# Performance work log

Measured on AMD Instinct MI355X. Metric: run time of the kernel, lower is better.

## Reference

```python
import jax, jax.numpy as jnp
import numpy as np

N_NODES = 50000
N_EDGES = 800000
IN_C = 32
HID = 64
N_LAYERS = 3
EDGE_HID = 128
OUT_C = 1
N_GRAPHS = 8


def setup_inputs() -> dict:
    key = jax.random.key(0)
    ks = jax.random.split(key, 32)
    x = jax.random.normal(ks[0], (N_NODES, IN_C), dtype=jnp.float32)
    # edges with src != dst so that PyG's remove_self_loops is a no-op
    src = jax.random.randint(ks[1], (N_EDGES,), 0, N_NODES)
    off = jax.random.randint(ks[2], (N_EDGES,), 1, N_NODES)
    dst = (src + off) % N_NODES
    edge_index = jnp.stack([src, dst]).astype(jnp.int32)
    batch = jnp.sort(jax.random.randint(ks[3], (N_NODES,), 0, N_GRAPHS)).astype(jnp.int32)
    inp = {"x": x, "edge_index": edge_index, "batch": batch}
    i = 4
    for l in range(N_LAYERS):
        din = IN_C if l == 0 else HID
        s = 1.0 / float(np.sqrt(din))
        inp[f"Wl{l}"] = jax.random.normal(ks[i], (din, HID), dtype=jnp.float32) * s; i += 1
        inp[f"bl{l}"] = jnp.zeros((HID,), jnp.float32)
        inp[f"Wr{l}"] = jax.random.normal(ks[i], (din, HID), dtype=jnp.float32) * s; i += 1
        inp[f"br{l}"] = jnp.zeros((HID,), jnp.float32)
        inp[f"att{l}"] = jax.random.normal(ks[i], (HID,), dtype=jnp.float32) * (1.0 / float(np.sqrt(HID))); i += 1
        inp[f"res{l}"] = jax.random.normal(ks[i], (din, HID), dtype=jnp.float32) * s; i += 1
        inp[f"bias{l}"] = jnp.zeros((HID,), jnp.float32)
        inp[f"lng{l}"] = jnp.ones((HID,), jnp.float32)
        inp[f"lnb{l}"] = jnp.zeros((HID,), jnp.float32)
    efd = 3 * HID
    inp["W1"] = jax.random.normal(ks[i], (efd, EDGE_HID), dtype=jnp.float32) * (1.0 / float(np.sqrt(efd))); i += 1
    inp["b1"] = jnp.zeros((EDGE_HID,), jnp.float32)
    inp["W2"] = jax.random.normal(ks[i], (EDGE_HID, OUT_C), dtype=jnp.float32) * (1.0 / float(np.sqrt(EDGE_HID))); i += 1
    inp["b2"] = jnp.zeros((OUT_C,), jnp.float32)
    return inp


def _gatv2_layer(x, src, dst, Wl, bl, Wr, br, att, resW, bias):
    # GATv2Conv (heads=1, share_weights=False, residual=True, add_self_loops handled by caller)
    n = x.shape[0]
    xl = x @ Wl + bl  # source transform  [N, C]
    xr = x @ Wr + br  # target transform  [N, C]
    e = jax.nn.leaky_relu(xl[src] + xr[dst], 0.2)  # [E, C]
    logits = e @ att                               # [E]
    m = jax.ops.segment_max(logits, dst, num_segments=n)
    ex = jnp.exp(logits - m[dst])
    denom = jax.ops.segment_sum(ex, dst, num_segments=n)
    alpha = ex / denom[dst]                        # edge softmax over incoming edges
    out = jax.ops.segment_sum(alpha[:, None] * xl[src], dst, num_segments=n)
    return out + x @ resW + bias


def _layernorm(h, g, b):
    mu = h.mean(-1, keepdims=True)
    var = h.var(-1, keepdims=True)
    return (h - mu) * jax.lax.rsqrt(var + 1e-5) * g + b


def reference(x, edge_index, batch,
              Wl0, bl0, Wr0, br0, att0, res0, bias0, lng0, lnb0,
              Wl1, bl1, Wr1, br1, att1, res1, bias1, lng1, lnb1,
              Wl2, bl2, Wr2, br2, att2, res2, bias2, lng2, lnb2,
              W1, b1, W2, b2):
    n = x.shape[0]
    loop = jnp.arange(n, dtype=edge_index.dtype)
    src = jnp.concatenate([edge_index[0], loop])  # add self loops
    dst = jnp.concatenate([edge_index[1], loop])
    layers = [(Wl0, bl0, Wr0, br0, att0, res0, bias0, lng0, lnb0),
              (Wl1, bl1, Wr1, br1, att1, res1, bias1, lng1, lnb1),
              (Wl2, bl2, Wr2, br2, att2, res2, bias2, lng2, lnb2)]
    h = x
    for (Wl, bl, Wr, br, att, resW, bias, g, b) in layers:
        h = _gatv2_layer(h, src, dst, Wl, bl, Wr, br, att, resW, bias)
        h = jax.nn.relu(_layernorm(h, g, b))
    node_repr = h
    gc = jax.ops.segment_sum(node_repr, batch, num_segments=N_GRAPHS)  # global_add_pool
    s, d = edge_index[0], edge_index[1]
    edge_feat = jnp.concatenate([node_repr[s], node_repr[d], gc[batch[s]]], axis=-1)  # [E, 3*HID]
    return jax.nn.relu(edge_feat @ W1 + b1) @ W2 + b2
```

## Files before the change

kernel.cpp:

```cpp
#include <hip/hip_runtime.h>
#include <math.h>

typedef float floatx2 __attribute__((ext_vector_type(2)));
typedef float floatx4 __attribute__((ext_vector_type(4)));
typedef short bf16x8 __attribute__((ext_vector_type(8)));
typedef _Float16 halfx2 __attribute__((ext_vector_type(2)));

#define NODE_MASK 0x07FFFFFF
#define LOG2E 1.4426950408889634f

__device__ __forceinline__ float wave_sum(float v){
#pragma unroll
  for (int m = 1; m < 64; m <<= 1) v += __shfl_xor(v, m, 64);
  return v;
}

__device__ __forceinline__ unsigned short bf16_of(float a){
  unsigned ua = __float_as_uint(a);
  ua = (ua + 0x7FFFu + ((ua >> 16) & 1u)) >> 16;
  return (unsigned short)ua;
}
__device__ __forceinline__ unsigned pack_bf16(float a, float b){
  unsigned ua = __float_as_uint(a), ub = __float_as_uint(b);
  ua = (ua + 0x7FFFu + ((ua >> 16) & 1u)) >> 16;
  ub = (ub + 0x7FFFu + ((ub >> 16) & 1u)) >> 16;
  return ua | (ub << 16);
}
__device__ __forceinline__ float2 unpack_bf16(unsigned p){
  float2 r;
  r.x = __uint_as_float(p << 16);
  r.y = __uint_as_float(p & 0xFFFF0000u);
  return r;
}
__device__ __forceinline__ bf16x8 to_bf16x8(float4 a, float4 b){
  bf16x8 r;
  r[0]=(short)bf16_of(a.x); r[1]=(short)bf16_of(a.y);
  r[2]=(short)bf16_of(a.z); r[3]=(short)bf16_of(a.w);
  r[4]=(short)bf16_of(b.x); r[5]=(short)bf16_of(b.y);
  r[6]=(short)bf16_of(b.z); r[7]=(short)bf16_of(b.w);
  return r;
}
__device__ __forceinline__ halfx2 f22h2(float a, float b){
  auto r = __builtin_amdgcn_cvt_pkrtz(a, b);
  return *(halfx2*)&r;
}
__device__ __forceinline__ float fdot2h(halfx2 a, halfx2 b, float c){
  return __builtin_amdgcn_fdot2(a, b, c, false);
}

__global__ void k_deg_rank(const int* __restrict__ dst, int* __restrict__ deg,
                           int* __restrict__ rank, int e){
  int i = (blockIdx.x*blockDim.x + threadIdx.x) * 4;
  if (i + 3 < e){
    int4 d4 = *(const int4*)&dst[i];
    int4 r4;
    r4.x = atomicAdd(&deg[d4.x], 1);
    r4.y = atomicAdd(&deg[d4.y], 1);
    r4.z = atomicAdd(&deg[d4.z], 1);
    r4.w = atomicAdd(&deg[d4.w], 1);
    *(int4*)&rank[i] = r4;
  } else {
    for (int j = i; j < e; ++j) rank[j] = atomicAdd(&deg[dst[j]], 1);
  }
}

__global__ void k_scan_a(const int* __restrict__ deg, int* __restrict__ rowptr,
                         int* __restrict__ bsum, int n){
  __shared__ int sm[256];
  int i = blockIdx.x*256 + threadIdx.x;
  int v = (i < n) ? (deg[i] + 1) : 0;
  sm[threadIdx.x] = v; __syncthreads();
#pragma unroll
  for (int off = 1; off < 256; off <<= 1){
    int t = (threadIdx.x >= off) ? sm[threadIdx.x - off] : 0;
    __syncthreads();
    sm[threadIdx.x] += t;
    __syncthreads();
  }
  if (i < n) rowptr[i] = sm[threadIdx.x] - v;
  if (threadIdx.x == 255) bsum[blockIdx.x] = sm[255];
}

__global__ void k_scan_b(int* __restrict__ bsum, int* __restrict__ rowptr, int nb, int n){
  __shared__ int sm[256];
  int t = threadIdx.x;
  int v = (t < nb) ? bsum[t] : 0;
  sm[t] = v; __syncthreads();
#pragma unroll
  for (int off = 1; off < 256; off <<= 1){
    int x = (t >= off) ? sm[t - off] : 0;
    __syncthreads();
    sm[t] += x;
    __syncthreads();
  }
  if (t < nb) bsum[t] = sm[t] - v;
  if (t == 255) rowptr[n] = sm[255];
}

__global__ void k_scan_c_selfloop(int* __restrict__ rowptr, const int* __restrict__ bsum,
                                  int* __restrict__ csr,
                                  const int* __restrict__ batch,
                                  float* __restrict__ gc, int n){
  int i = blockIdx.x*256 + threadIdx.x;
  if (i < n){
    int r = rowptr[i] + bsum[blockIdx.x];
    rowptr[i] = r;
    csr[r] = i | (batch[i] << 27);
  }
  if (blockIdx.x == 0){
    gc[threadIdx.x] = 0.f;
    gc[threadIdx.x + 256] = 0.f;
  }
}

__global__ void k_scatter(const int* __restrict__ src, const int* __restrict__ dst,
                          const int* __restrict__ batch,
                          const int* __restrict__ rowptr, const int* __restrict__ rank,
                          int* __restrict__ csr, int* __restrict__ eidA, int e){
  int i = (blockIdx.x*blockDim.x + threadIdx.x) * 4;
  if (i + 3 < e){
    int4 s4 = *(const int4*)&src[i];
    int4 d4 = *(const int4*)&dst[i];
    int4 r4 = *(const int4*)&rank[i];
    int p0 = rowptr[d4.x] + 1 + r4.x;
    int p1 = rowptr[d4.y] + 1 + r4.y;
    int p2 = rowptr[d4.z] + 1 + r4.z;
    int p3 = rowptr[d4.w] + 1 + r4.w;
    csr[p0] = s4.x | (batch[s4.x] << 27);
    csr[p1] = s4.y | (batch[s4.y] << 27);
    csr[p2] = s4.z | (batch[s4.z] << 27);
    csr[p3] = s4.w | (batch[s4.w] << 27);
    eidA[p0] = i;
    eidA[p1] = i + 1;
    eidA[p2] = i + 2;
    eidA[p3] = i + 3;
  } else {
    for (int j = i; j < e; ++j){
      int d = dst[j], sv = src[j];
      int pos = rowptr[d] + 1 + rank[j];
      csr[pos] = sv | (batch[sv] << 27);
      eidA[pos] = j;
    }
  }
}

template<int K>
__global__ __launch_bounds__(256)
void k_node_transform(const float* __restrict__ h,
                      const float* __restrict__ Wl, const float* __restrict__ bl,
                      const float* __restrict__ Wr, const float* __restrict__ br,
                      const float* __restrict__ Wres, const float* __restrict__ bias,
                      unsigned short* __restrict__ xl8, float* __restrict__ xr,
                      float* __restrict__ res, int n){
  const int KH = K / 32;
  int lane = threadIdx.x & 63;
  int nt   = threadIdx.x >> 6;
  int nn = lane & 15, q = lane >> 4;
  int m0 = blockIdx.x * 64;
  if (m0 >= n) return;
  bf16x8 Af[4][KH];
#pragma unroll
  for (int t = 0; t < 4; ++t){
#pragma unroll
    for (int kh = 0; kh < KH; ++kh){
      int node = min(m0 + t*16 + nn, n - 1);
      const float* hp = h + (size_t)node*K + kh*32 + q*8;
      Af[t][kh] = to_bf16x8(*(const float4*)hp, *(const float4*)(hp + 4));
    }
  }
  int n0 = nt * 16;
  for (int sel = 0; sel < 3; ++sel){
    const float* Wp = (sel == 0) ? Wl : (sel == 1) ? Wr : Wres;
    const float* bp = (sel == 0) ? bl : (sel == 1) ? br : bias;
    bf16x8 Bf[KH];
#pragma unroll
    for (int kh = 0; kh < KH; ++kh){
#pragma unroll
      for (int j = 0; j < 8; ++j)
        Bf[kh][j] = (short)bf16_of(Wp[(kh*32 + q*8 + j)*64 + n0 + nn]);
    }
    float bv = bp[n0 + nn];
#pragma unroll
    for (int t = 0; t < 4; ++t){
      floatx4 acc = {bv, bv, bv, bv};
#pragma unroll
      for (int kh = 0; kh < KH; ++kh)
        acc = __builtin_amdgcn_mfma_f32_16x16x32_bf16(Af[t][kh], Bf[kh], acc, 0, 0, 0);
      int nodeb = m0 + t*16 + q*4;
      if (sel == 0){
#pragma unroll
        for (int reg = 0; reg < 4; ++reg){
          float v = acc[reg];
          float p = __shfl_xor(v, 1, 64);
          int node = nodeb + reg;
          if (!(nn & 1) && node < n)
            xl8[(size_t)node*32 + ((n0 + nn) >> 1)] =
              (unsigned short)__builtin_amdgcn_cvt_pk_fp8_f32(v, p, 0, false);
        }
      } else {
        float* op = (sel == 1) ? xr : res;
#pragma unroll
        for (int reg = 0; reg < 4; ++reg){
          int node = nodeb + reg;
          if (node < n) op[(size_t)node*64 + n0 + nn] = acc[reg];
        }
      }
    }
  }
}

__global__ void k_gat_edge(const uint2* __restrict__ xl_u2, const float* __restrict__ xr,
                           const float* __restrict__ att,
                           const float* __restrict__ lng, const float* __restrict__ lnb,
                           const int* __restrict__ rowptr, const int* __restrict__ csr,
                           float* __restrict__ hio, int n){
  int node = (blockIdx.x*blockDim.x + threadIdx.x) >> 6;
  int lane = threadIdx.x & 63;
  if (node >= n) return;
  int sub = lane >> 3;
  int l   = lane & 7;
  size_t base = (size_t)node*64 + 8*l;
  float4 xr0 = *(const float4*)&xr[base];
  float4 xr1 = *(const float4*)&xr[base + 4];
  float4 at0f = *(const float4*)&att[8*l];
  float4 at1f = *(const float4*)&att[8*l + 4];
  halfx2 xh0 = f22h2(xr0.x, xr0.y), xh1 = f22h2(xr0.z, xr0.w);
  halfx2 xh2 = f22h2(xr1.x, xr1.y), xh3 = f22h2(xr1.z, xr1.w);
  halfx2 at0 = f22h2(at0f.x*LOG2E, at0f.y*LOG2E);
  halfx2 at1 = f22h2(at0f.z*LOG2E, at0f.w*LOG2E);
  halfx2 at2 = f22h2(at1f.x*LOG2E, at1f.y*LOG2E);
  halfx2 at3 = f22h2(at1f.z*LOG2E, at1f.w*LOG2E);
  halfx2 z2  = {(_Float16)0.f, (_Float16)0.f};
  halfx2 c02 = {(_Float16)0.2f, (_Float16)0.2f};
  int p0 = rowptr[node], p1 = rowptr[node+1];
  int deg = p1 - p0;
  int sreg = csr[p0 + min(lane, deg-1)];
  int rounds = (deg + 7) >> 3;
  float dsum = 0.f;
  float a0=0.f,a1=0.f,a2=0.f,a3=0.f,a4=0.f,a5=0.f,a6=0.f,a7=0.f;
  int e0 = sub;
  bool v0 = e0 < deg;
  int s0 = __shfl(sreg, v0 ? e0 : 0, 64) & NODE_MASK;
  uint2 x0 = xl_u2[(size_t)s0*8 + l];
  int e1 = 8 + sub;
  bool v1 = e1 < deg;
  uint2 x1 = x0;
  if (rounds > 1){
    int s1 = __shfl(sreg, v1 ? e1 : 0, 64) & NODE_MASK;
    x1 = xl_u2[(size_t)s1*8 + l];
  }
  for (int r = 0; r < rounds; ++r){
    int en = 8*(r+2) + sub;
    bool vn = en < deg;
    uint2 xn = x0;
    if (r + 2 < rounds){
      int sn;
      if (en < 64) sn = __shfl(sreg, vn ? en : 0, 64);
      else         sn = csr[p0 + (vn ? en : 0)];
      sn &= NODE_MASK;
      xn = xl_u2[(size_t)sn*8 + l];
    }
    floatx2 p01 = __builtin_amdgcn_cvt_pk_f32_fp8(x0.x, false);
    floatx2 p23 = __builtin_amdgcn_cvt_pk_f32_fp8(x0.x, true);
    floatx2 p45 = __builtin_amdgcn_cvt_pk_f32_fp8(x0.y, false);
    floatx2 p67 = __builtin_amdgcn_cvt_pk_f32_fp8(x0.y, true);
    halfx2 v0h = f22h2(p01.x, p01.y) + xh0;
    halfx2 v1h = f22h2(p23.x, p23.y) + xh1;
    halfx2 v2h = f22h2(p45.x, p45.y) + xh2;
    halfx2 v3h = f22h2(p67.x, p67.y) + xh3;
    halfx2 lr0 = __builtin_elementwise_min(v0h, z2) * c02 + __builtin_elementwise_max(v0h, z2);
    halfx2 lr1 = __builtin_elementwise_min(v1h, z2) * c02 + __builtin_elementwise_max(v1h, z2);
    halfx2 lr2 = __builtin_elementwise_min(v2h, z2) * c02 + __builtin_elementwise_max(v2h, z2);
    halfx2 lr3 = __builtin_elementwise_min(v3h, z2) * c02 + __builtin_elementwise_max(v3h, z2);
    float partial = fdot2h(lr3, at3, fdot2h(lr2, at2, fdot2h(lr1, at1, fdot2h(lr0, at0, 0.f))));
#pragma unroll
    for (int mm = 1; mm < 8; mm <<= 1) partial += __shfl_xor(partial, mm, 64);
    float w = v0 ? exp2f(partial) : 0.f;
    dsum += w;
    a0 = fmaf(w, p01.x, a0);
    a1 = fmaf(w, p01.y, a1);
    a2 = fmaf(w, p23.x, a2);
    a3 = fmaf(w, p23.y, a3);
    a4 = fmaf(w, p45.x, a4);
    a5 = fmaf(w, p45.y, a5);
    a6 = fmaf(w, p67.x, a6);
    a7 = fmaf(w, p67.y, a7);
    x0 = x1; v0 = v1;
    x1 = xn; v1 = vn;
  }
#pragma unroll
  for (int off = 8; off < 64; off <<= 1){
    dsum += __shfl_xor(dsum, off, 64);
    a0 += __shfl_xor(a0, off, 64);
    a1 += __shfl_xor(a1, off, 64);
    a2 += __shfl_xor(a2, off, 64);
    a3 += __shfl_xor(a3, off, 64);
    a4 += __shfl_xor(a4, off, 64);
    a5 += __shfl_xor(a5, off, 64);
    a6 += __shfl_xor(a6, off, 64);
    a7 += __shfl_xor(a7, off, 64);
  }
  float4 r0 = *(const float4*)&hio[base];
  float4 r1 = *(const float4*)&hio[base + 4];
  float inv = __builtin_amdgcn_rcpf(dsum);
  float o0 = fmaf(a0, inv, r0.x);
  float o1 = fmaf(a1, inv, r0.y);
  float o2 = fmaf(a2, inv, r0.z);
  float o3 = fmaf(a3, inv, r0.w);
  float o4 = fmaf(a4, inv, r1.x);
  float o5 = fmaf(a5, inv, r1.y);
  float o6 = fmaf(a6, inv, r1.z);
  float o7 = fmaf(a7, inv, r1.w);
  float mean = wave_sum(o0+o1+o2+o3+o4+o5+o6+o7) * (1.f/512.f);
  float d0 = o0-mean, d1 = o1-mean, d2 = o2-mean, d3 = o3-mean;
  float d4 = o4-mean, d5 = o5-mean, d6 = o6-mean, d7 = o7-mean;
  float var = wave_sum(d0*d0+d1*d1+d2*d2+d3*d3+d4*d4+d5*d5+d6*d6+d7*d7) * (1.f/512.f);
  float rstd = rsqrtf(var + 1e-5f);
  if (sub == 0){
    float4 lg0 = *(const float4*)&lng[8*l];
    float4 lg1 = *(const float4*)&lng[8*l + 4];
    float4 lb0 = *(const float4*)&lnb[8*l];
    float4 lb1 = *(const float4*)&lnb[8*l + 4];
    float4 out0, out1;
    out0.x = fmaxf(fmaf(d0*rstd, lg0.x, lb0.x), 0.f);
    out0.y = fmaxf(fmaf(d1*rstd, lg0.y, lb0.y), 0.f);
    out0.z = fmaxf(fmaf(d2*rstd, lg0.z, lb0.z), 0.f);
    out0.w = fmaxf(fmaf(d3*rstd, lg0.w, lb0.w), 0.f);
    out1.x = fmaxf(fmaf(d4*rstd, lg1.x, lb1.x), 0.f);
    out1.y = fmaxf(fmaf(d5*rstd, lg1.y, lb1.y), 0.f);
    out1.z = fmaxf(fmaf(d6*rstd, lg1.z, lb1.z), 0.f);
    out1.w = fmaxf(fmaf(d7*rstd, lg1.w, lb1.w), 0.f);
    *(float4*)&hio[base] = out0;
    *(float4*)&hio[base + 4] = out1;
  }
}

__global__ void k_pool(const float* __restrict__ h, const int* __restrict__ batch,
                       float* __restrict__ gc, int n){
  int wid  = (blockIdx.x*blockDim.x + threadIdx.x) >> 6;
  int lane = threadIdx.x & 63;
  int n0 = wid*64;
  if (n0 >= n) return;
  int n1 = min(n0+64, n);
  int curg = batch[n0];
  float s = 0.f;
  for (int i = n0; i < n1; ++i){
    int g = batch[i];
    if (g != curg){ atomicAdd(&gc[curg*64+lane], s); s = 0.f; curg = g; }
    s += h[(size_t)i*64 + lane];
  }
  atomicAdd(&gc[curg*64+lane], s);
}

__global__ void k_graph_proj(const float* __restrict__ gc, const float* __restrict__ W1,
                             const float* __restrict__ b1, unsigned* __restrict__ Gh){
  int g = threadIdx.x >> 7;
  int j = threadIdx.x & 127;
  float a = b1[j];
#pragma unroll 8
  for (int k = 0; k < 64; ++k) a = fmaf(gc[g*64+k], W1[(128+k)*128 + j], a);
  float p = __shfl_xor(a, 1, 64);
  if (!(j & 1)){
    halfx2 hv = f22h2(a, p);
    Gh[g*64 + (j >> 1)] = *(unsigned*)&hv;
  }
}

__global__ __launch_bounds__(256)
void k_node_proj(const float* __restrict__ nr, const float* __restrict__ W1,
                 unsigned short* __restrict__ Au16, unsigned* __restrict__ Bu, int n){
  int lane = threadIdx.x & 63;
  int wave = threadIdx.x >> 6;
  int nn = lane & 15, q = lane >> 4;
  int m0 = blockIdx.x * 64;
  if (m0 >= n) return;
  bf16x8 Af[4][2];
#pragma unroll
  for (int t = 0; t < 4; ++t){
#pragma unroll
    for (int kh = 0; kh < 2; ++kh){
      int node = min(m0 + t*16 + nn, n - 1);
      const float* hp = nr + (size_t)node*64 + kh*32 + q*8;
      Af[t][kh] = to_bf16x8(*(const float4*)hp, *(const float4*)(hp + 4));
    }
  }
  for (int half = 0; half < 2; ++half){
#pragma unroll
    for (int ni = 0; ni < 2; ++ni){
      int nt = wave + ni*4;
      int n0 = nt * 16;
      bf16x8 Bf[2];
#pragma unroll
      for (int kh = 0; kh < 2; ++kh){
#pragma unroll
        for (int j = 0; j < 8; ++j)
          Bf[kh][j] = (short)bf16_of(W1[(half*64 + kh*32 + q*8 + j)*128 + n0 + nn]);
      }
#pragma unroll
      for (int t = 0; t < 4; ++t){
        floatx4 acc = {0.f, 0.f, 0.f, 0.f};
#pragma unroll
        for (int kh = 0; kh < 2; ++kh)
          acc = __builtin_amdgcn_mfma_f32_16x16x32_bf16(Af[t][kh], Bf[kh], acc, 0, 0, 0);
        int nodeb = m0 + t*16 + q*4;
#pragma unroll
        for (int reg = 0; reg < 4; ++reg){
          float v = acc[reg];
          float p = __shfl_xor(v, 1, 64);
          int node = nodeb + reg;
          if (!(nn & 1) && node < n){
            int j = (n0 + nn) >> 1;
            if (half == 0)
              Au16[(size_t)node*64 + j] =
                (unsigned short)__builtin_amdgcn_cvt_pk_fp8_f32(v, p, 0, false);
            else
              Bu[(size_t)node*64 + j] = pack_bf16(v, p);
          }
        }
      }
    }
  }
}

__global__ void k_edge_out_csr(const uint4* __restrict__ Au4, const uint4* __restrict__ Bu4,
                               const unsigned* __restrict__ Gh,
                               const int* __restrict__ rowptr, const int* __restrict__ csr,
                               const int* __restrict__ eidA,
                               const float* __restrict__ W2, const float* __restrict__ b2,
                               float* __restrict__ out, int n){
  int node = (blockIdx.x*blockDim.x + threadIdx.x) >> 6;
  int lane = threadIdx.x & 63;
  if (node >= n) return;
  int sub = lane >> 3;
  int l   = lane & 7;
  int p0 = rowptr[node];
  int deg2 = rowptr[node+1] - p0 - 1;
  if (deg2 <= 0) return;
  int idx = p0 + 1 + min(lane, deg2-1);
  int sreg = csr[idx];
  int ereg = eidA[idx];
  uint4 ba = Bu4[(size_t)node*16 + 2*l];
  uint4 bb = Bu4[(size_t)node*16 + 2*l + 1];
  float2 t0 = unpack_bf16(ba.x), t1 = unpack_bf16(ba.y);
  float2 t2 = unpack_bf16(ba.z), t3 = unpack_bf16(ba.w);
  float2 t4 = unpack_bf16(bb.x), t5 = unpack_bf16(bb.y);
  float2 t6 = unpack_bf16(bb.z), t7 = unpack_bf16(bb.w);
  halfx2 bh0 = f22h2(t0.x, t0.y), bh1 = f22h2(t1.x, t1.y);
  halfx2 bh2 = f22h2(t2.x, t2.y), bh3 = f22h2(t3.x, t3.y);
  halfx2 bh4 = f22h2(t4.x, t4.y), bh5 = f22h2(t5.x, t5.y);
  halfx2 bh6 = f22h2(t6.x, t6.y), bh7 = f22h2(t7.x, t7.y);
  float4 w0 = *(const float4*)&W2[16*l];
  float4 w1 = *(const float4*)&W2[16*l + 4];
  float4 w2 = *(const float4*)&W2[16*l + 8];
  float4 w3 = *(const float4*)&W2[16*l + 12];
  halfx2 wh0 = f22h2(w0.x, w0.y), wh1 = f22h2(w0.z, w0.w);
  halfx2 wh2 = f22h2(w1.x, w1.y), wh3 = f22h2(w1.z, w1.w);
  halfx2 wh4 = f22h2(w2.x, w2.y), wh5 = f22h2(w2.z, w2.w);
  halfx2 wh6 = f22h2(w3.x, w3.y), wh7 = f22h2(w3.z, w3.w);
  halfx2 z2 = {(_Float16)0.f, (_Float16)0.f};
  float b2v = b2[0];
  int rounds = (deg2 + 7) >> 3;
  int e0 = sub;
  bool v0 = e0 < deg2;
  int q0 = v0 ? e0 : 0;
  int c0 = __shfl(sreg, q0, 64);
  int id0 = __shfl(ereg, q0, 64);
  uint4 A0 = Au4[(size_t)(c0 & NODE_MASK)*8 + l];
  int e1 = 8 + sub;
  bool v1 = e1 < deg2;
  int c1 = c0, id1 = id0; uint4 A1 = A0;
  if (rounds > 1){
    int q1 = v1 ? e1 : 0;
    c1 = __shfl(sreg, q1, 64);
    id1 = __shfl(ereg, q1, 64);
    A1 = Au4[(size_t)(c1 & NODE_MASK)*8 + l];
  }
  for (int r = 0; r < rounds; ++r){
    int en = 8*(r+2) + sub;
    bool vn = en < deg2;
    int cn = c0, idn = id0; uint4 An = A0;
    if (r + 2 < rounds){
      int qn = vn ? en : 0;
      if (en < 64){ cn = __shfl(sreg, qn, 64); idn = __shfl(ereg, qn, 64); }
      else        { cn = csr[p0 + 1 + qn];     idn = eidA[p0 + 1 + qn]; }
      An = Au4[(size_t)(cn & NODE_MASK)*8 + l];
    }
    int g = ((unsigned)c0) >> 27;
    const uint4* gp = (const uint4*)(Gh + g*64 + 8*l);
    uint4 g0 = gp[0], g1 = gp[1];
    halfx2 gh0 = *(halfx2*)&g0.x, gh1 = *(halfx2*)&g0.y;
    halfx2 gh2 = *(halfx2*)&g0.z, gh3 = *(halfx2*)&g0.w;
    halfx2 gh4 = *(halfx2*)&g1.x, gh5 = *(halfx2*)&g1.y;
    halfx2 gh6 = *(halfx2*)&g1.z, gh7 = *(halfx2*)&g1.w;
    floatx2 a01 = __builtin_amdgcn_cvt_pk_f32_fp8(A0.x, false);
    floatx2 a23 = __builtin_amdgcn_cvt_pk_f32_fp8(A0.x, true);
    floatx2 a45 = __builtin_amdgcn_cvt_pk_f32_fp8(A0.y, false);
    floatx2 a67 = __builtin_amdgcn_cvt_pk_f32_fp8(A0.y, true);
    floatx2 a89 = __builtin_amdgcn_cvt_pk_f32_fp8(A0.z, false);
    floatx2 aab = __builtin_amdgcn_cvt_pk_f32_fp8(A0.z, true);
    floatx2 acd = __builtin_amdgcn_cvt_pk_f32_fp8(A0.w, false);
    floatx2 aef = __builtin_amdgcn_cvt_pk_f32_fp8(A0.w, true);
    halfx2 h0 = __builtin_elementwise_max(f22h2(a01.x, a01.y) + bh0 + gh0, z2);
    halfx2 h1 = __builtin_elementwise_max(f22h2(a23.x, a23.y) + bh1 + gh1, z2);
    halfx2 h2 = __builtin_elementwise_max(f22h2(a45.x, a45.y) + bh2 + gh2, z2);
    halfx2 h3 = __builtin_elementwise_max(f22h2(a67.x, a67.y) + bh3 + gh3, z2);
    halfx2 h4 = __builtin_elementwise_max(f22h2(a89.x, a89.y) + bh4 + gh4, z2);
    halfx2 h5 = __builtin_elementwise_max(f22h2(aab.x, aab.y) + bh5 + gh5, z2);
    halfx2 h6 = __builtin_elementwise_max(f22h2(acd.x, acd.y) + bh6 + gh6, z2);
    halfx2 h7 = __builtin_elementwise_max(f22h2(aef.x, aef.y) + bh7 + gh7, z2);
    float part = fdot2h(h7, wh7, fdot2h(h6, wh6, fdot2h(h5, wh5, fdot2h(h4, wh4,
                 fdot2h(h3, wh3, fdot2h(h2, wh2, fdot2h(h1, wh1, fdot2h(h0, wh0, 0.f))))))));
#pragma unroll
    for (int mm = 1; mm < 8; mm <<= 1) part += __shfl_xor(part, mm, 64);
    if (l == 0 && v0) out[id0] = part + b2v;
    c0 = c1; id0 = id1; A0 = A1; v0 = v1;
    c1 = cn; id1 = idn; A1 = An; v1 = vn;
  }
}

extern "C" void kernel_launch(void* const* d_in, const int* in_sizes, int n_in,
                              void* d_out, int out_size, void* d_ws, size_t ws_size,
                              hipStream_t stream){
  const float* x     = (const float*)d_in[0];
  const int*   ei    = (const int*)d_in[1];
  const int*   batch = (const int*)d_in[2];
  const int N = in_sizes[2];
  const int E = in_sizes[1] / 2;
  const int* src = ei;
  const int* dst = ei + E;

  unsigned* W = (unsigned*)d_ws;
  const size_t N16 = (size_t)N * 16;
  const size_t N32 = (size_t)N * 32;
  const size_t N64 = (size_t)N * 64;
  unsigned short* xl8 = (unsigned short*)W;
  float* xr = (float*)(W + N16);
  float* hE = (float*)(W + N16 + N64);
  float* hD = (float*)(W + N16 + 2*N64);
  unsigned short* Au16 = (unsigned short*)W;
  unsigned* Bu = W + N32;
  int* rowptr = (int*)(W + N16 + 3*N64);
  int* deg    = rowptr + (N + 16);
  int* csr    = deg + N;
  int* rank   = csr + (N + E);
  int* eidA   = rank + E;
  float* gc   = (float*)(eidA + (N + E));
  unsigned* Gh = (unsigned*)(gc + 512);
  int* bsum   = (int*)(Gh + 512);

  const int NB = (N + 255) / 256;
  const int NT64 = (N + 63) / 64;

  (void)hipMemsetAsync(deg, 0, (size_t)N*4, stream);
  k_deg_rank <<<(E/4+255)/256, 256, 0, stream>>>(dst, deg, rank, E);
  k_scan_a   <<<NB, 256, 0, stream>>>(deg, rowptr, bsum, N);
  k_scan_b   <<<1, 256, 0, stream>>>(bsum, rowptr, NB, N);
  k_scan_c_selfloop<<<NB, 256, 0, stream>>>(rowptr, bsum, csr, batch, gc, N);
  k_scatter  <<<(E/4+255)/256, 256, 0, stream>>>(src, dst, batch, rowptr, rank, csr, eidA, E);

  const float* h = x;
  float* hn = hD;
  for (int l = 0; l < 3; ++l){
    const float* Wl   = (const float*)d_in[3 + 9*l + 0];
    const float* bl   = (const float*)d_in[3 + 9*l + 1];
    const float* Wr   = (const float*)d_in[3 + 9*l + 2];
    const float* br   = (const float*)d_in[3 + 9*l + 3];
    const float* att  = (const float*)d_in[3 + 9*l + 4];
    const float* Wres = (const float*)d_in[3 + 9*l + 5];
    const float* bias = (const float*)d_in[3 + 9*l + 6];
    const float* lng  = (const float*)d_in[3 + 9*l + 7];
    const float* lnb  = (const float*)d_in[3 + 9*l + 8];
    if (l == 0)
      k_node_transform<32><<<NT64, 256, 0, stream>>>(h, Wl, bl, Wr, br, Wres, bias, xl8, xr, hn, N);
    else
      k_node_transform<64><<<NT64, 256, 0, stream>>>(h, Wl, bl, Wr, br, Wres, bias, xl8, xr, hn, N);
    k_gat_edge<<<(N+3)/4, 256, 0, stream>>>((const uint2*)xl8, xr, att, lng, lnb, rowptr, csr, hn, N);
    h = hn;
    hn = (l == 0) ? hE : hD;
  }

  const float* W1 = (const float*)d_in[30];
  const float* b1 = (const float*)d_in[31];
  const float* W2 = (const float*)d_in[32];
  const float* b2 = (const float*)d_in[33];

  int pool_waves = (N + 63) / 64;
  k_pool      <<<(pool_waves+3)/4, 256, 0, stream>>>(hD, batch, gc, N);
  k_graph_proj<<<1, 1024, 0, stream>>>(gc, W1, b1, Gh);
  k_node_proj <<<NT64, 256, 0, stream>>>(hD, W1, Au16, Bu, N);
  k_edge_out_csr<<<(N+3)/4, 256, 0, stream>>>((const uint4*)Au16, (const uint4*)Bu, Gh,
                                              rowptr, csr, eidA, W2, b2, (float*)d_out, N);
}
```

Measured before the change: 421.2 us.

## Merge scan kernels into reduce-then-apply and fuse pooling into node projection

Replaces the three-kernel exclusive scan with two kernels. The first reduces each block's degree sum using wave shuffles, and the second has every block redo the small block-sum prefix itself and apply it together with the local scan and self-loop CSR writes. The separate pooling kernel is folded into the node-projection launch as extra blocks, with batch ids loaded once per wave and read by shuffle. Graph projection is relaunched as 8 blocks of 128 threads. This removes kernel launches and serialization points, at the cost of redundant per-block prefix work and a heterogeneous fused kernel.

```diff
diff --git a/kernel.cpp b/kernel.cpp
--- a/kernel.cpp
+++ b/kernel.cpp
@@ -64,27 +64,37 @@
   }
 }
 
-__global__ void k_scan_a(const int* __restrict__ deg, int* __restrict__ rowptr,
-                         int* __restrict__ bsum, int n){
-  __shared__ int sm[256];
+__global__ void k_scan_reduce(const int* __restrict__ deg, int* __restrict__ bsum, int n){
+  __shared__ int sm[4];
   int i = blockIdx.x*256 + threadIdx.x;
   int v = (i < n) ? (deg[i] + 1) : 0;
-  sm[threadIdx.x] = v; __syncthreads();
-#pragma unroll
-  for (int off = 1; off < 256; off <<= 1){
-    int t = (threadIdx.x >= off) ? sm[threadIdx.x - off] : 0;
-    __syncthreads();
-    sm[threadIdx.x] += t;
-    __syncthreads();
-  }
-  if (i < n) rowptr[i] = sm[threadIdx.x] - v;
-  if (threadIdx.x == 255) bsum[blockIdx.x] = sm[255];
-}
-
-__global__ void k_scan_b(int* __restrict__ bsum, int* __restrict__ rowptr, int nb, int n){
+#pragma unroll
+  for (int m = 1; m < 64; m <<= 1) v += __shfl_xor(v, m, 64);
+  if ((threadIdx.x & 63) == 0) sm[threadIdx.x >> 6] = v;
+  __syncthreads();
+  if (threadIdx.x == 0) bsum[blockIdx.x] = sm[0] + sm[1] + sm[2] + sm[3];
+}
+
+__global__ void k_scan_apply(const int* __restrict__ deg, const int* __restrict__ bsum,
+                             int* __restrict__ rowptr, int* __restrict__ csr,
+                             const int* __restrict__ batch, float* __restrict__ gc,
+                             int n, int nb){
+  __shared__ int pre[256];
   __shared__ int sm[256];
   int t = threadIdx.x;
-  int v = (t < nb) ? bsum[t] : 0;
+  int b = blockIdx.x;
+  int pv = (t < nb) ? bsum[t] : 0;
+  pre[t] = pv; __syncthreads();
+#pragma unroll
+  for (int off = 1; off < 256; off <<= 1){
+    int x = (t >= off) ? pre[t - off] : 0;
+    __syncthreads();
+    pre[t] += x;
+    __syncthreads();
+  }
+  int P = (b > 0) ? pre[b - 1] : 0;
+  int i = b*256 + t;
+  int v = (i < n) ? (deg[i] + 1) : 0;
   sm[t] = v; __syncthreads();
 #pragma unroll
   for (int off = 1; off < 256; off <<= 1){
@@ -93,23 +103,15 @@
     sm[t] += x;
     __syncthreads();
   }
-  if (t < nb) bsum[t] = sm[t] - v;
-  if (t == 255) rowptr[n] = sm[255];
-}
-
-__global__ void k_scan_c_selfloop(int* __restrict__ rowptr, const int* __restrict__ bsum,
-                                  int* __restrict__ csr,
-                                  const int* __restrict__ batch,
-                                  float* __restrict__ gc, int n){
-  int i = blockIdx.x*256 + threadIdx.x;
   if (i < n){
-    int r = rowptr[i] + bsum[blockIdx.x];
+    int r = P + sm[t] - v;
     rowptr[i] = r;
     csr[r] = i | (batch[i] << 27);
   }
-  if (blockIdx.x == 0){
-    gc[threadIdx.x] = 0.f;
-    gc[threadIdx.x + 256] = 0.f;
+  if (b == nb - 1 && t == 255) rowptr[n] = P + sm[255];
+  if (b == 0){
+    gc[t] = 0.f;
+    gc[t + 256] = 0.f;
   }
 }
 
@@ -335,27 +337,10 @@
   }
 }
 
-__global__ void k_pool(const float* __restrict__ h, const int* __restrict__ batch,
-                       float* __restrict__ gc, int n){
-  int wid  = (blockIdx.x*blockDim.x + threadIdx.x) >> 6;
-  int lane = threadIdx.x & 63;
-  int n0 = wid*64;
-  if (n0 >= n) return;
-  int n1 = min(n0+64, n);
-  int curg = batch[n0];
-  float s = 0.f;
-  for (int i = n0; i < n1; ++i){
-    int g = batch[i];
-    if (g != curg){ atomicAdd(&gc[curg*64+lane], s); s = 0.f; curg = g; }
-    s += h[(size_t)i*64 + lane];
-  }
-  atomicAdd(&gc[curg*64+lane], s);
-}
-
 __global__ void k_graph_proj(const float* __restrict__ gc, const float* __restrict__ W1,
                              const float* __restrict__ b1, unsigned* __restrict__ Gh){
-  int g = threadIdx.x >> 7;
-  int j = threadIdx.x & 127;
+  int g = blockIdx.x;
+  int j = threadIdx.x;
   float a = b1[j];
 #pragma unroll 8
   for (int k = 0; k < 64; ++k) a = fmaf(gc[g*64+k], W1[(128+k)*128 + j], a);
@@ -367,13 +352,46 @@
 }
 
 __global__ __launch_bounds__(256)
-void k_node_proj(const float* __restrict__ nr, const float* __restrict__ W1,
-                 unsigned short* __restrict__ Au16, unsigned* __restrict__ Bu, int n){
+void k_node_proj_pool(const float* __restrict__ nr, const float* __restrict__ W1,
+                      const int* __restrict__ batch,
+                      unsigned short* __restrict__ Au16, unsigned* __restrict__ Bu,
+                      float* __restrict__ gc, int n, int nt64){
   int lane = threadIdx.x & 63;
   int wave = threadIdx.x >> 6;
+  if ((int)blockIdx.x >= nt64){
+    int wid = (blockIdx.x - nt64)*4 + wave;
+    int n0 = wid*64;
+    if (n0 >= n) return;
+    int n1 = min(n0 + 64, n);
+    int last = n1 - 1 - n0;
+    int bt = batch[min(n0 + lane, n - 1)];
+    int curg = __shfl(bt, 0, 64);
+    float s = 0.f;
+#pragma unroll
+    for (int bb = 0; bb < 64; bb += 8){
+      if (bb > last) break;
+      float v0_ = (bb+0 <= last) ? nr[(size_t)(n0+bb+0)*64 + lane] : 0.f;
+      float v1_ = (bb+1 <= last) ? nr[(size_t)(n0+bb+1)*64 + lane] : 0.f;
+      float v2_ = (bb+2 <= last) ? nr[(size_t)(n0+bb+2)*64 + lane] : 0.f;
+      float v3_ = (bb+3 <= last) ? nr[(size_t)(n0+bb+3)*64 + lane] : 0.f;
+      float v4_ = (bb+4 <= last) ? nr[(size_t)(n0+bb+4)*64 + lane] : 0.f;
+      float v5_ = (bb+5 <= last) ? nr[(size_t)(n0+bb+5)*64 + lane] : 0.f;
+      float v6_ = (bb+6 <= last) ? nr[(size_t)(n0+bb+6)*64 + lane] : 0.f;
+      float v7_ = (bb+7 <= last) ? nr[(size_t)(n0+bb+7)*64 + lane] : 0.f;
+#pragma unroll
+      for (int j = 0; j < 8; ++j){
+        int g = __shfl(bt, min(bb + j, last), 64);
+        if (g != curg){ atomicAdd(&gc[curg*64 + lane], s); s = 0.f; curg = g; }
+        float vj = (j==0)?v0_:(j==1)?v1_:(j==2)?v2_:(j==3)?v3_:
+                   (j==4)?v4_:(j==5)?v5_:(j==6)?v6_:v7_;
+        s += vj;
+      }
+    }
+    atomicAdd(&gc[curg*64 + lane], s);
+    return;
+  }
   int nn = lane & 15, q = lane >> 4;
   int m0 = blockIdx.x * 64;
-  if (m0 >= n) return;
   bf16x8 Af[4][2];
 #pragma unroll
   for (int t = 0; t < 4; ++t){
@@ -552,11 +570,10 @@
   const int NT64 = (N + 63) / 64;
 
   (void)hipMemsetAsync(deg, 0, (size_t)N*4, stream);
-  k_deg_rank <<<(E/4+255)/256, 256, 0, stream>>>(dst, deg, rank, E);
-  k_scan_a   <<<NB, 256, 0, stream>>>(deg, rowptr, bsum, N);
-  k_scan_b   <<<1, 256, 0, stream>>>(bsum, rowptr, NB, N);
-  k_scan_c_selfloop<<<NB, 256, 0, stream>>>(rowptr, bsum, csr, batch, gc, N);
-  k_scatter  <<<(E/4+255)/256, 256, 0, stream>>>(src, dst, batch, rowptr, rank, csr, eidA, E);
+  k_deg_rank   <<<(E/4+255)/256, 256, 0, stream>>>(dst, deg, rank, E);
+  k_scan_reduce<<<NB, 256, 0, stream>>>(deg, bsum, N);
+  k_scan_apply <<<NB, 256, 0, stream>>>(deg, bsum, rowptr, csr, batch, gc, N, NB);
+  k_scatter    <<<(E/4+255)/256, 256, 0, stream>>>(src, dst, batch, rowptr, rank, csr, eidA, E);
 
   const float* h = x;
   float* hn = hD;
@@ -585,9 +602,9 @@
   const float* b2 = (const float*)d_in[33];
 
   int pool_waves = (N + 63) / 64;
-  k_pool      <<<(pool_waves+3)/4, 256, 0, stream>>>(hD, batch, gc, N);
-  k_graph_proj<<<1, 1024, 0, stream>>>(gc, W1, b1, Gh);
-  k_node_proj <<<NT64, 256, 0, stream>>>(hD, W1, Au16, Bu, N);
+  int poolB = (pool_waves + 3) / 4;
+  k_node_proj_pool<<<NT64 + poolB, 256, 0, stream>>>(hD, W1, batch, Au16, Bu, gc, N, NT64);
+  k_graph_proj<<<8, 128, 0, stream>>>(gc, W1, b1, Gh);
   k_edge_out_csr<<<(N+3)/4, 256, 0, stream>>>((const uint4*)Au16, (const uint4*)Bu, Gh,
                                               rowptr, csr, eidA, W2, b2, (float*)d_out, N);
 }
```

Measured after the change: 391.2 us. 1.08x faster.
